# Kernel optimization log

Hardware: AMD Instinct MI355X
Metric: run time of the kernel (lower is better)

## Reference

```python
import jax, jax.numpy as jnp
import numpy as np

B, L = 8, 128
STATE_DIM, ACT_DIM = 6, 3
E = 256
D_MODEL = 256
N_LAYER = 4
D_INNER = 512   # expand=2
D_STATE = 16
DT_RANK = 16    # ceil(d_model/16)
D_CONV = 4
MAX_EP_LEN = 300
EPS = 1e-5


def rmsnorm(x, w):
    return x * jax.lax.rsqrt(jnp.mean(x * x, axis=-1, keepdims=True) + EPS) * w


def mamba_mixer(x, in_W, conv_w, conv_b, xproj_W, dt_W, dt_b, A_log, Dp, out_W):
    # x: (B, Lp, D_MODEL)
    bsz, Lp, _ = x.shape
    di = conv_w.shape[0]
    n = A_log.shape[-1]
    rk = dt_W.shape[0]
    xz = x @ in_W                              # (B, Lp, 2*di)
    xc, z = jnp.split(xz, 2, axis=-1)
    # depthwise causal conv1d, kernel D_CONV
    xc_t = xc.transpose(0, 2, 1)               # (B, di, Lp)
    xc_t = jax.lax.conv_general_dilated(
        xc_t, conv_w[:, None, :], (1,), [(D_CONV - 1, 0)],
        feature_group_count=di,
        dimension_numbers=('NCH', 'OIH', 'NCH')) + conv_b[None, :, None]
    xc = jax.nn.silu(xc_t.transpose(0, 2, 1))  # (B, Lp, di)
    proj = xc @ xproj_W                        # (B, Lp, rk + 2n)
    dt, Bm, Cm = jnp.split(proj, [rk, rk + n], axis=-1)
    dt = jax.nn.softplus(dt @ dt_W + dt_b)     # (B, Lp, di)
    A = -jnp.exp(A_log)                        # (di, n)

    def step(h, inp):
        dt_t, B_t, C_t, x_t = inp              # (B,di),(B,n),(B,n),(B,di)
        dA = jnp.exp(dt_t[:, :, None] * A)     # (B, di, n)
        h = dA * h + (dt_t * x_t)[:, :, None] * B_t[:, None, :]
        y = jnp.einsum('bdn,bn->bd', h, C_t)
        return h, y

    h0 = jnp.zeros((bsz, di, n), x.dtype)
    _, ys = jax.lax.scan(step, h0, (dt.transpose(1, 0, 2), Bm.transpose(1, 0, 2),
                                    Cm.transpose(1, 0, 2), xc.transpose(1, 0, 2)))
    y = ys.transpose(1, 0, 2) + xc * Dp        # (B, Lp, di)
    y = y * jax.nn.silu(z)
    return y @ out_W


def setup_inputs():
    key = jax.random.key(0)
    ks = jax.random.split(key, 24)
    s = 0.05
    inp = {}
    inp['states'] = jax.random.normal(ks[0], (B, L, STATE_DIM), jnp.float32)
    inp['actions'] = jax.random.normal(ks[1], (B, L, ACT_DIM), jnp.float32)
    inp['goal'] = jax.random.normal(ks[2], (B, L, STATE_DIM), jnp.float32)
    inp['timesteps'] = jax.random.randint(ks[3], (B, L), 0, MAX_EP_LEN)
    inp['te_W'] = jax.random.normal(ks[4], (MAX_EP_LEN, E)) * 0.02
    inp['se_W'] = jax.random.normal(ks[5], (STATE_DIM, E)) * s
    inp['se_b'] = jnp.zeros((E,))
    inp['ge_W'] = jax.random.normal(ks[6], (STATE_DIM, E)) * s
    inp['ge_b'] = jnp.zeros((E,))
    inp['ae_W'] = jax.random.normal(ks[7], (ACT_DIM, E)) * s
    inp['ae_b'] = jnp.zeros((E,))
    inp['bb_in_W'] = jax.random.normal(ks[8], (E, D_MODEL)) * s
    inp['bb_in_b'] = jnp.zeros((D_MODEL,))
    inp['norm_w'] = jnp.ones((N_LAYER, D_MODEL))
    inp['in_proj_W'] = jax.random.normal(ks[9], (N_LAYER, D_MODEL, 2 * D_INNER)) * s
    inp['conv_w'] = jax.random.normal(ks[10], (N_LAYER, D_INNER, D_CONV)) * s
    inp['conv_b'] = jnp.zeros((N_LAYER, D_INNER))
    inp['xproj_W'] = jax.random.normal(ks[11], (N_LAYER, D_INNER, DT_RANK + 2 * D_STATE)) * s
    inp['dt_W'] = jax.random.normal(ks[12], (N_LAYER, DT_RANK, D_INNER)) * s
    inp['dt_b'] = jnp.full((N_LAYER, D_INNER), float(np.log(np.expm1(0.01))), jnp.float32)
    inp['A_log'] = jnp.log(jnp.tile(jnp.arange(1, D_STATE + 1, dtype=jnp.float32), (N_LAYER, D_INNER, 1)))
    inp['Dp'] = jnp.ones((N_LAYER, D_INNER))
    inp['out_W'] = jax.random.normal(ks[13], (N_LAYER, D_INNER, D_MODEL)) * s / np.sqrt(N_LAYER)
    inp['fnorm_w'] = jnp.ones((D_MODEL,))
    inp['ps_W'] = jax.random.normal(ks[14], (D_MODEL, STATE_DIM)) * s
    inp['ps_b'] = jnp.zeros((STATE_DIM,))
    inp['pa_W'] = jax.random.normal(ks[15], (D_MODEL, ACT_DIM)) * s
    inp['pa_b'] = jnp.zeros((ACT_DIM,))
    return inp


def reference(states, actions, goal, timesteps, te_W, se_W, se_b, ge_W, ge_b,
              ae_W, ae_b, bb_in_W, bb_in_b, norm_w, in_proj_W, conv_w, conv_b,
              xproj_W, dt_W, dt_b, A_log, Dp, out_W, fnorm_w, ps_W, ps_b, pa_W, pa_b):
    bsz, Ls, _ = states.shape
    se = states @ se_W + se_b
    ge = goal @ ge_W + ge_b
    ae = actions @ ae_W + ae_b
    te = te_W[timesteps]                       # (B, L, E)
    se = se + te
    ae = ae + te
    ge = ge + te
    # interleave (g, s, a) per timestep -> (B, 3L, E)
    u = jnp.stack((ge, se, ae), axis=1).transpose(0, 2, 1, 3).reshape(bsz, 3 * Ls, E)
    residual = u @ bb_in_W + bb_in_b
    for i in range(norm_w.shape[0]):
        xn = rmsnorm(residual, norm_w[i])
        residual = residual + mamba_mixer(xn, in_proj_W[i], conv_w[i], conv_b[i],
                                          xproj_W[i], dt_W[i], dt_b[i], A_log[i],
                                          Dp[i], out_W[i])
    y = rmsnorm(residual, fnorm_w)
    y = y.reshape(bsz, Ls, 3, y.shape[-1]).transpose(0, 2, 1, 3)  # (B, 3, L, D)
    state_preds = y[:, -1] @ ps_W + ps_b       # from action-slot tokens
    action_preds = jnp.tanh(y[:, -2] @ pa_W + pa_b)  # from state-slot tokens
    return (state_preds, action_preds)
```

## Files before the change

### kernel.cpp

```cpp
#include <hip/hip_runtime.h>
#include <hip/hip_bf16.h>
#include <math.h>

#define BB 8
#define LL 128
#define SS 384
#define BT 3072
#define EE 256
#define DM 256
#define DI 512
#define DSTATE 16
#define RK 16
#define NL 4

typedef unsigned short u16;
typedef __attribute__((ext_vector_type(8))) short short8;
typedef __attribute__((ext_vector_type(4))) float f32x4;

__device__ __forceinline__ float bf(const u16 v){
    union { unsigned u; float f; } c; c.u = ((unsigned)v) << 16; return c.f;
}
__device__ __forceinline__ u16 f2bf(float f){
    union { float f; unsigned u; } c; c.f = f;
    unsigned x = c.u;
    unsigned r = (x >> 16) & 1u;
    x += 0x7fffu + r;
    return (u16)(x >> 16);
}
__device__ __forceinline__ unsigned pack2(float a, float b){
    return ((unsigned)f2bf(a)) | (((unsigned)f2bf(b)) << 16);
}

__global__ void k_probe(const unsigned* __restrict__ norm_w_raw, int* __restrict__ flag){
    if (threadIdx.x == 0 && blockIdx.x == 0){
        *flag = (norm_w_raw[0] == 0x3F800000u) ? 0 : 1;
    }
}

struct CvtArgs {
    const void* src[27];
    int n[27];
    int off[27];
};

__global__ __launch_bounds__(256) void k_convert(CvtArgs a, const int* __restrict__ flag,
                                                 float* __restrict__ dst){
    const int f = *flag;
    const int stride = gridDim.x * blockDim.x;
    const int tid0 = blockIdx.x * blockDim.x + threadIdx.x;
    #pragma unroll 1
    for (int s = 0; s < 27; ++s){
        const int n = a.n[s];
        float* d = dst + a.off[s];
        if (f){
            const u16* p = (const u16*)a.src[s];
            for (int i = tid0; i < n; i += stride) d[i] = bf(p[i]);
        } else {
            const float* p = (const float*)a.src[s];
            for (int i = tid0; i < n; i += stride) d[i] = p[i];
        }
    }
}

struct SwzDesc { const float* src; u16* dst; int K; int N; int frags; };
struct SwzArgs { SwzDesc d[13]; };

__global__ __launch_bounds__(256) void k_swz(SwzArgs a){
    int gid = blockIdx.x*256 + threadIdx.x;
    #pragma unroll 1
    for (int s = 0; s < 13; ++s){
        int f = a.d[s].frags;
        if (gid < f){
            const float* src = a.d[s].src;
            const int K = a.d[s].K, N = a.d[s].N;
            const int l = gid & 63;
            const int rest = gid >> 6;
            const int kcn = K >> 5;
            const int kc = rest % kcn;
            const int nt = rest / kcn;
            const int n  = nt*16 + (l & 15);
            const int k0 = kc*32 + (l >> 4)*8;
            u16 tmp[8];
            #pragma unroll
            for (int j = 0; j < 8; ++j) tmp[j] = f2bf(src[(size_t)(k0+j)*N + n]);
            *(short8*)(a.d[s].dst + (size_t)gid*8) = *(short8*)tmp;
            return;
        }
        gid -= f;
    }
}

__global__ __launch_bounds__(256) void k_embed_mfma(
    const float* __restrict__ states, const float* __restrict__ actions,
    const float* __restrict__ goal, const int* __restrict__ tsteps,
    const float* __restrict__ te_W, const float* __restrict__ se_W, const float* __restrict__ se_b,
    const float* __restrict__ ge_W, const float* __restrict__ ge_b,
    const float* __restrict__ ae_W, const float* __restrict__ ae_b,
    const u16* __restrict__ bbsw, const float* __restrict__ bb_b,
    float* __restrict__ residual)
{
    __shared__ u16 sA[32*264];
    const int tid = threadIdx.x;
    {
        const int m = tid >> 3, p = tid & 7, e0 = p*32;
        const int token = blockIdx.x*32 + m;
        const int b = token / SS, t = token % SS;
        const int slot = t % 3, step = t / 3;
        const int ts = tsteps[b*LL + step];
        float v[32];
        const float* tp = te_W + ts*EE + e0;
        #pragma unroll
        for (int i = 0; i < 8; ++i) *(float4*)(&v[i*4]) = *(const float4*)(tp + i*4);
        const float *bias, *Wp, *g; int nk;
        if (slot == 0){ bias = ge_b; Wp = ge_W; g = goal    + (b*LL+step)*6; nk = 6; }
        else if (slot == 1){ bias = se_b; Wp = se_W; g = states + (b*LL+step)*6; nk = 6; }
        else { bias = ae_b; Wp = ae_W; g = actions + (b*LL+step)*3; nk = 3; }
        #pragma unroll
        for (int i = 0; i < 8; ++i){
            float4 bv = *(const float4*)(bias + e0 + i*4);
            v[i*4]+=bv.x; v[i*4+1]+=bv.y; v[i*4+2]+=bv.z; v[i*4+3]+=bv.w;
        }
        for (int k = 0; k < nk; ++k){
            float gv = g[k];
            const float* wr = Wp + k*EE + e0;
            #pragma unroll
            for (int i = 0; i < 8; ++i){
                float4 wv = *(const float4*)(wr + i*4);
                v[i*4]+=gv*wv.x; v[i*4+1]+=gv*wv.y; v[i*4+2]+=gv*wv.z; v[i*4+3]+=gv*wv.w;
            }
        }
        unsigned* dp = (unsigned*)sA + (m*264 + e0)/2;
        #pragma unroll
        for (int i = 0; i < 16; ++i) dp[i] = pack2(v[2*i], v[2*i+1]);
    }
    __syncthreads();
    const int w = tid >> 6, l = tid & 63;
    const int mt = w >> 1, nq = w & 1;
    f32x4 acc[4] = {{0,0,0,0},{0,0,0,0},{0,0,0,0},{0,0,0,0}};
    const u16* ap0 = sA + (mt*16 + (l&15))*264 + (l>>4)*8;
    #pragma unroll
    for (int kc = 0; kc < 8; ++kc){
        short8 a = *(const short8*)(ap0 + kc*32);
        #pragma unroll
        for (int nt = 0; nt < 4; ++nt){
            int ntg = blockIdx.y*8 + nq*4 + nt;
            short8 b8 = *(const short8*)(bbsw + ((size_t)(ntg*8 + kc)*64 + l)*8);
            acc[nt] = __builtin_amdgcn_mfma_f32_16x16x32_bf16(a, b8, acc[nt], 0,0,0);
        }
    }
    const int mrow0 = blockIdx.x*32 + mt*16 + (l>>4)*4;
    #pragma unroll
    for (int nt = 0; nt < 4; ++nt){
        int col = (blockIdx.y*8 + nq*4 + nt)*16 + (l&15);
        float bb = bb_b[col];
        #pragma unroll
        for (int r = 0; r < 4; ++r)
            residual[(mrow0+r)*DM + col] = acc[nt][r] + bb;
    }
}

__global__ __launch_bounds__(256) void k_rms_inproj_mfma(
    const float* __restrict__ residual, const float* __restrict__ norm_w,
    const u16* __restrict__ Wsw,
    float* __restrict__ xc_raw, float* __restrict__ sz)
{
    __shared__ u16 sA[32*264];
    const int tid = threadIdx.x;
    {
        const int m = tid >> 3, p = tid & 7, e0 = p*32;
        const int row = blockIdx.x*32 + m;
        float v[32];
        const float* rp = residual + row*DM + e0;
        #pragma unroll
        for (int i = 0; i < 8; ++i) *(float4*)(&v[i*4]) = *(const float4*)(rp + i*4);
        float s = 0.f;
        #pragma unroll
        for (int i = 0; i < 32; ++i) s += v[i]*v[i];
        s += __shfl_xor(s,1,64); s += __shfl_xor(s,2,64); s += __shfl_xor(s,4,64);
        const float scale = rsqrtf(s*(1.f/DM) + 1e-5f);
        const float* nwp = norm_w + e0;
        unsigned* dp = (unsigned*)sA + (m*264 + e0)/2;
        #pragma unroll
        for (int i = 0; i < 16; ++i)
            dp[i] = pack2(v[2*i]*scale*nwp[2*i], v[2*i+1]*scale*nwp[2*i+1]);
    }
    __syncthreads();
    const int w = tid >> 6, l = tid & 63;
    const int mt = w >> 1, nq = w & 1;
    f32x4 acc[4] = {{0,0,0,0},{0,0,0,0},{0,0,0,0},{0,0,0,0}};
    const u16* ap0 = sA + (mt*16 + (l&15))*264 + (l>>4)*8;
    #pragma unroll
    for (int kc = 0; kc < 8; ++kc){
        short8 a = *(const short8*)(ap0 + kc*32);
        #pragma unroll
        for (int nt = 0; nt < 4; ++nt){
            int ntg = blockIdx.y*8 + nq*4 + nt;
            short8 b8 = *(const short8*)(Wsw + ((size_t)(ntg*8 + kc)*64 + l)*8);
            acc[nt] = __builtin_amdgcn_mfma_f32_16x16x32_bf16(a, b8, acc[nt], 0,0,0);
        }
    }
    const int mrow0 = blockIdx.x*32 + mt*16 + (l>>4)*4;
    if (blockIdx.y < 4){
        #pragma unroll
        for (int nt = 0; nt < 4; ++nt){
            int col = (blockIdx.y*8 + nq*4 + nt)*16 + (l&15);
            #pragma unroll
            for (int r = 0; r < 4; ++r)
                xc_raw[(mrow0+r)*DI + col] = acc[nt][r];
        }
    } else {
        #pragma unroll
        for (int nt = 0; nt < 4; ++nt){
            int col = (blockIdx.y*8 + nq*4 + nt)*16 + (l&15) - DI;
            #pragma unroll
            for (int r = 0; r < 4; ++r){
                float z = acc[nt][r];
                sz[(mrow0+r)*DI + col] = z / (1.f + __expf(-z));
            }
        }
    }
}

__global__ __launch_bounds__(256) void k_conv_mfma(
    const float* __restrict__ xc_raw,
    const float* __restrict__ conv_w, const float* __restrict__ conv_b,
    const u16* __restrict__ xpsw,
    const float* __restrict__ dt_W, const float* __restrict__ dt_b,
    float* __restrict__ xc, float* __restrict__ dtBC, float* __restrict__ dt)
{
    __shared__ u16 sxc[16*520];
    __shared__ float sdtbc[16*64];
    const int tid = threadIdx.x;
    const int base = blockIdx.x * 16;
    const int t0 = base % SS;

    #pragma unroll
    for (int half = 0; half < 2; ++half){
        const int d = tid + half*256;
        const float w0 = conv_w[d*4+0], w1 = conv_w[d*4+1];
        const float w2 = conv_w[d*4+2], w3 = conv_w[d*4+3];
        const float cb = conv_b[d];
        const float* rp = xc_raw + (size_t)base*DI + d;
        float xm3=0.f, xm2=0.f, xm1=0.f;
        if (t0 > 0){
            xm3 = rp[-3*DI]; xm2 = rp[-2*DI]; xm1 = rp[-DI];
        }
        #pragma unroll
        for (int tk = 0; tk < 16; ++tk){
            float x0 = rp[tk*DI];
            float a = cb + w0*xm3 + w1*xm2 + w2*xm1 + w3*x0;
            float s = a / (1.f + __expf(-a));
            xc[(size_t)(base+tk)*DI + d] = s;
            sxc[tk*520 + d] = f2bf(s);
            xm3 = xm2; xm2 = xm1; xm1 = x0;
        }
    }
    __syncthreads();

    const int w = tid >> 6, l = tid & 63;
    if (w < 3){
        f32x4 acc = {0,0,0,0};
        const u16* ap0 = sxc + (l&15)*520 + (l>>4)*8;
        #pragma unroll
        for (int kc = 0; kc < 16; ++kc){
            short8 a = *(const short8*)(ap0 + kc*32);
            short8 b8 = *(const short8*)(xpsw + ((size_t)(w*16 + kc)*64 + l)*8);
            acc = __builtin_amdgcn_mfma_f32_16x16x32_bf16(a, b8, acc, 0,0,0);
        }
        #pragma unroll
        for (int r = 0; r < 4; ++r)
            sdtbc[((l>>4)*4 + r)*64 + w*16 + (l&15)] = acc[r];
    }
    __syncthreads();

    #pragma unroll
    for (int r = 0; r < 2; ++r){
        int i = tid + r*256;
        int t = i >> 5, j = i & 31;
        dtBC[(size_t)(base+t)*48 + 16 + j] = sdtbc[t*64 + 16 + j];
    }

    #pragma unroll
    for (int half = 0; half < 2; ++half){
        const int d = tid + half*256;
        const float db = dt_b[d];
        float wr[16];
        #pragma unroll
        for (int r = 0; r < 16; ++r) wr[r] = dt_W[r*DI + d];
        #pragma unroll
        for (int tk = 0; tk < 16; ++tk){
            float a = db;
            #pragma unroll
            for (int r = 0; r < 16; ++r) a += sdtbc[tk*64 + r] * wr[r];
            float sp = (a > 15.f) ? a : __logf(1.f + __expf(a));
            dt[(size_t)(base+tk)*DI + d] = sp;
        }
    }
}

#define CT 32
#define NCH (SS/CT)

__global__ __launch_bounds__(256) void k_scan(
    const float* __restrict__ dt, const float* __restrict__ dtBC,
    const float* __restrict__ xc,
    const float* __restrict__ A_log, const float* __restrict__ Dp,
    float* __restrict__ y)
{
    __shared__ float s_dt[2][CT*16];
    __shared__ float s_xc[2][CT*16];
    __shared__ float s_B [2][CT*16];
    __shared__ float s_C [2][CT*16];
    __shared__ float s_p [CT*16*17];
    __shared__ float s_Dp[16];

    const int tid = threadIdx.x;
    const int bk  = blockIdx.x;
    const int b   = bk >> 5;
    const int dg  = bk & 31;
    const int dgb = dg*16;
    const int ld  = tid >> 4, n = tid & 15;
    const int d   = dgb + ld;

    const float A = -__expf(A_log[d*DSTATE + n]);
    const size_t tokbase = (size_t)b*SS;

    float r_dt[2], r_xc[2], r_bc[4];

    auto issue_loads = [&](int c){
        const int t0 = c*CT;
        #pragma unroll
        for (int r = 0; r < 2; ++r){
            int e = tid + r*256;
            int t = e >> 4, dd = e & 15;
            size_t g = (tokbase + t0 + t)*DI + dgb + dd;
            r_dt[r] = dt[g];
            r_xc[r] = xc[g];
        }
        #pragma unroll
        for (int r = 0; r < 4; ++r){
            int e = tid + r*256;
            int t = e >> 5, j = e & 31;
            r_bc[r] = dtBC[(tokbase + t0 + t)*48 + 16 + j];
        }
    };
    auto commit = [&](int bu){
        #pragma unroll
        for (int r = 0; r < 2; ++r){
            int e = tid + r*256;
            s_dt[bu][e] = r_dt[r];
            s_xc[bu][e] = r_xc[r];
        }
        #pragma unroll
        for (int r = 0; r < 4; ++r){
            int e = tid + r*256;
            int t = e >> 5, j = e & 31;
            if (j < 16) s_B[bu][t*16 + j]      = r_bc[r];
            else        s_C[bu][t*16 + (j-16)] = r_bc[r];
        }
    };

    issue_loads(0);
    commit(0);
    if (tid < 16) s_Dp[tid] = Dp[dgb + tid];

    float h = 0.f;
    int buf = 0;
    for (int c = 0; c < NCH; ++c){
        __syncthreads();
        if (c+1 < NCH) issue_loads(c+1);
        const float* pdt = s_dt[buf];
        const float* pxc = s_xc[buf];
        const float* pB  = s_B[buf];
        const float* pC  = s_C[buf];
        float* pp = s_p + ld*17 + n;
        #pragma unroll
        for (int t = 0; t < CT; ++t){
            float dtv = pdt[t*16 + ld];
            float xv  = pxc[t*16 + ld];
            float Bv  = pB [t*16 + n];
            float dA  = __expf(dtv * A);
            h = dA*h + (dtv*xv)*Bv;
            pp[t*272] = h * pC[t*16 + n];
        }
        __syncthreads();
        {
            const int t0 = c*CT;
            #pragma unroll
            for (int r = 0; r < 2; ++r){
                int e = tid + r*256;
                int t = e >> 4, dd = e & 15;
                const float* q = s_p + e*17;
                float s = 0.f;
                #pragma unroll
                for (int k = 0; k < 16; ++k) s += q[k];
                y[(tokbase + t0 + t)*DI + dgb + dd] = s + pxc[e]*s_Dp[dd];
            }
        }
        if (c+1 < NCH) commit(buf^1);
        buf ^= 1;
    }
}

__global__ __launch_bounds__(256) void k_outproj_mfma(
    const float* __restrict__ y, const float* __restrict__ szb,
    const u16* __restrict__ Wsw, float* __restrict__ residual)
{
    __shared__ u16 sA[16*520];
    const int tid = threadIdx.x;
    {
        const int m = tid >> 4, p = tid & 15, e0 = p*32;
        const int row = blockIdx.x*16 + m;
        const float* yp = y   + (size_t)row*DI + e0;
        const float* sp = szb + (size_t)row*DI + e0;
        unsigned* dp = (unsigned*)sA + (m*520 + e0)/2;
        #pragma unroll
        for (int i = 0; i < 8; ++i){
            float4 yv = *(const float4*)(yp + i*4);
            float4 sv = *(const float4*)(sp + i*4);
            dp[i*2]   = pack2(yv.x*sv.x, yv.y*sv.y);
            dp[i*2+1] = pack2(yv.z*sv.z, yv.w*sv.w);
        }
    }
    __syncthreads();
    const int w = tid >> 6, l = tid & 63;
    f32x4 acc[2] = {{0,0,0,0},{0,0,0,0}};
    const u16* ap0 = sA + (l&15)*520 + (l>>4)*8;
    #pragma unroll
    for (int kc = 0; kc < 16; ++kc){
        short8 a = *(const short8*)(ap0 + kc*32);
        #pragma unroll
        for (int i = 0; i < 2; ++i){
            int ntg = blockIdx.y*8 + w*2 + i;
            short8 b8 = *(const short8*)(Wsw + ((size_t)(ntg*16 + kc)*64 + l)*8);
            acc[i] = __builtin_amdgcn_mfma_f32_16x16x32_bf16(a, b8, acc[i], 0,0,0);
        }
    }
    const int mrow0 = blockIdx.x*16 + (l>>4)*4;
    #pragma unroll
    for (int i = 0; i < 2; ++i){
        int col = (blockIdx.y*8 + w*2 + i)*16 + (l&15);
        #pragma unroll
        for (int r = 0; r < 4; ++r)
            residual[(mrow0+r)*DM + col] += acc[i][r];
    }
}

__global__ __launch_bounds__(256) void k_heads(
    const float* __restrict__ residual, const float* __restrict__ fnorm_w,
    const float* __restrict__ ps_W, const float* __restrict__ ps_b,
    const float* __restrict__ pa_W, const float* __restrict__ pa_b,
    const int* __restrict__ flag, void* __restrict__ out)
{
    __shared__ float x1[DM], x2[DM];
    __shared__ float sc[2];
    __shared__ float part[2][4];
    const int tid = threadIdx.x;
    const int bl = blockIdx.x;
    const int b = bl >> 7, l = bl & 127;
    const int fl = *flag;
    const int tok1 = b*SS + 3*l + 1;
    const int tok2 = tok1 + 1;
    float v1 = residual[tok1*DM + tid];
    float v2 = residual[tok2*DM + tid];
    {
        float s1 = v1*v1, s2 = v2*v2;
        #pragma unroll
        for (int off = 32; off >= 1; off >>= 1){
            s1 += __shfl_xor(s1, off, 64);
            s2 += __shfl_xor(s2, off, 64);
        }
        if ((tid & 63) == 0){ part[0][tid>>6] = s1; part[1][tid>>6] = s2; }
    }
    __syncthreads();
    if (tid < 2){
        float s = part[tid][0]+part[tid][1]+part[tid][2]+part[tid][3];
        sc[tid] = rsqrtf(s * (1.f/DM) + 1e-5f);
    }
    __syncthreads();
    float nw = fnorm_w[tid];
    x1[tid] = v1 * sc[0] * nw;
    x2[tid] = v2 * sc[1] * nw;
    __syncthreads();
    const int wv = tid >> 6, ln = tid & 63;
    for (int oi = wv; oi < 9; oi += 4){
        float a = 0.f;
        if (oi < 6){
            #pragma unroll
            for (int k = 0; k < 4; ++k){ int e = ln + 64*k; a += x2[e] * ps_W[e*6 + oi]; }
        } else {
            int j = oi - 6;
            #pragma unroll
            for (int k = 0; k < 4; ++k){ int e = ln + 64*k; a += x1[e] * pa_W[e*3 + j]; }
        }
        #pragma unroll
        for (int off = 32; off >= 1; off >>= 1) a += __shfl_xor(a, off, 64);
        if (ln == 0){
            float r; int idx;
            if (oi < 6){
                r = a + ps_b[oi];
                idx = (b*LL + l)*6 + oi;
            } else {
                int j = oi - 6;
                r = tanhf(a + pa_b[j]);
                idx = BB*LL*6 + (b*LL + l)*3 + j;
            }
            if (fl) ((u16*)out)[idx] = f2bf(r);
            else    ((float*)out)[idx] = r;
        }
    }
}

extern "C" void kernel_launch(void* const* d_in, const int* in_sizes, int n_in,
                              void* d_out, int out_size, void* d_ws, size_t ws_size,
                              hipStream_t stream)
{
    const int* tsteps = (const int*)d_in[3];

    int* flag = (int*)d_ws;
    float* fin = ((float*)d_ws) + 16;

    const int fidx[27] = {0,1,2,4,5,6,7,8,9,10,11,12,13,14,15,16,17,18,19,20,
                          21,22,23,24,25,26,27};
    CvtArgs ca;
    const float* fp[28];
    int cur = 0;
    for (int i = 0; i < 27; ++i){
        int gi = fidx[i];
        ca.src[i] = d_in[gi];
        ca.n[i]   = in_sizes[gi];
        ca.off[i] = cur;
        fp[gi] = fin + cur;
        cur += in_sizes[gi];
        cur = (cur + 3) & ~3;
    }
    float* act = fin + cur;

    float* residual = act;            act += BT*DM;
    float* xc_raw   = act;            act += BT*DI;
    float* sz       = act;            act += BT*DI;
    float* xc       = act;            act += BT*DI;
    float* dtbuf    = act;            act += BT*DI;
    float* ybuf     = act;            act += BT*DI;
    float* dtBC     = act;            act += BT*48;

    u16* wsb    = (u16*)act;
    u16* bb_sw  = wsb;
    u16* in_sw  = bb_sw + 65536;
    u16* out_sw = in_sw + 4*262144;
    u16* xp_sw  = out_sw + 4*131072;

    k_probe<<<1, 64, 0, stream>>>((const unsigned*)d_in[13], flag);
    k_convert<<<512, 256, 0, stream>>>(ca, flag, fin);

    SwzArgs sa;
    sa.d[0] = { fp[11], bb_sw, 256, 256, (256/16)*(256/32)*64 };
    for (int i = 0; i < 4; ++i)
        sa.d[1+i] = { fp[14] + i*DM*2*DI, in_sw + i*262144, 256, 1024,
                      (1024/16)*(256/32)*64 };
    for (int i = 0; i < 4; ++i)
        sa.d[5+i] = { fp[22] + i*DI*DM, out_sw + i*131072, 512, 256,
                      (256/16)*(512/32)*64 };
    for (int i = 0; i < 4; ++i)
        sa.d[9+i] = { fp[17] + i*DI*48, xp_sw + i*24576, 512, 48,
                      (48/16)*(512/32)*64 };
    int total_frags = 8192 + 4*32768 + 4*16384 + 4*3072;
    k_swz<<<total_frags/256, 256, 0, stream>>>(sa);

    k_embed_mfma<<<dim3(96,2), 256, 0, stream>>>(fp[0], fp[1], fp[2], tsteps,
        fp[4], fp[5], fp[6], fp[7], fp[8], fp[9], fp[10], bb_sw, fp[12], residual);

    for (int lyr = 0; lyr < NL; ++lyr){
        k_rms_inproj_mfma<<<dim3(96,8), 256, 0, stream>>>(residual, fp[13] + lyr*DM,
            in_sw + lyr*262144, xc_raw, sz);
        k_conv_mfma<<<BT/16, 256, 0, stream>>>(xc_raw, fp[15] + lyr*DI*4,
            fp[16] + lyr*DI, xp_sw + lyr*24576, fp[18] + lyr*RK*DI, fp[19] + lyr*DI,
            xc, dtBC, dtbuf);
        k_scan<<<256, 256, 0, stream>>>(dtbuf, dtBC, xc,
            fp[20] + lyr*DI*DSTATE, fp[21] + lyr*DI, ybuf);
        k_outproj_mfma<<<dim3(192,2), 256, 0, stream>>>(ybuf, sz,
            out_sw + lyr*131072, residual);
    }
    k_heads<<<BB*LL, 256, 0, stream>>>(residual, fp[23], fp[24], fp[25], fp[26], fp[27],
                                       flag, (u16*)d_out);
}
```

Before: 384.3 us.

## Fuse prep kernels and fold next-layer RMSNorm+in_proj into out_proj

Merges the dtype probe, input conversion and weight swizzle into one prep kernel. The swizzle now reads raw inputs directly, so weight matrices no longer get a separate fp32 conversion pass. The out-projection kernel now also applies the next layer's RMSNorm and in_proj (with SiLU on z) on its 16-row tile, which removes three inproj launches and a residual re-read. The scan stores dt and dt*x interleaved so the inner loop does one float2 load and one fewer multiply. The cost is that the fused kernel runs only 192 blocks for the full 1024-wide in_proj, so it has less parallelism than the separate 768-block launch.

```diff
diff --git a/kernel.cpp b/kernel.cpp
--- a/kernel.cpp
+++ b/kernel.cpp
@@ -30,63 +30,73 @@
 __device__ __forceinline__ unsigned pack2(float a, float b){
     return ((unsigned)f2bf(a)) | (((unsigned)f2bf(b)) << 16);
 }
-
-__global__ void k_probe(const unsigned* __restrict__ norm_w_raw, int* __restrict__ flag){
-    if (threadIdx.x == 0 && blockIdx.x == 0){
-        *flag = (norm_w_raw[0] == 0x3F800000u) ? 0 : 1;
-    }
-}
-
-struct CvtArgs {
-    const void* src[27];
-    int n[27];
-    int off[27];
+__device__ __forceinline__ int get_flag(const unsigned* nwraw){
+    return (nwraw[0] == 0x3F800000u) ? 0 : 1;
+}
+
+#define SWZ_NB 848
+#define CNV_NB 64
+
+__device__ __constant__ int g_soff[13] = {0, 0, 262144, 524288, 786432,
+                                          0, 131072, 262144, 393216,
+                                          0, 24576, 49152, 73728};
+
+struct SwzDesc { const void* src; u16* dst; int K; int N; int frags; };
+struct PrepArgs {
+    const void* csrc[23]; int cn[23]; int coff[23];
+    SwzDesc sd[13];
 };
 
-__global__ __launch_bounds__(256) void k_convert(CvtArgs a, const int* __restrict__ flag,
-                                                 float* __restrict__ dst){
-    const int f = *flag;
-    const int stride = gridDim.x * blockDim.x;
-    const int tid0 = blockIdx.x * blockDim.x + threadIdx.x;
-    #pragma unroll 1
-    for (int s = 0; s < 27; ++s){
-        const int n = a.n[s];
-        float* d = dst + a.off[s];
-        if (f){
-            const u16* p = (const u16*)a.src[s];
-            for (int i = tid0; i < n; i += stride) d[i] = bf(p[i]);
-        } else {
-            const float* p = (const float*)a.src[s];
-            for (int i = tid0; i < n; i += stride) d[i] = p[i];
-        }
-    }
-}
-
-struct SwzDesc { const float* src; u16* dst; int K; int N; int frags; };
-struct SwzArgs { SwzDesc d[13]; };
-
-__global__ __launch_bounds__(256) void k_swz(SwzArgs a){
-    int gid = blockIdx.x*256 + threadIdx.x;
-    #pragma unroll 1
-    for (int s = 0; s < 13; ++s){
-        int f = a.d[s].frags;
-        if (gid < f){
-            const float* src = a.d[s].src;
-            const int K = a.d[s].K, N = a.d[s].N;
-            const int l = gid & 63;
-            const int rest = gid >> 6;
-            const int kcn = K >> 5;
-            const int kc = rest % kcn;
-            const int nt = rest / kcn;
-            const int n  = nt*16 + (l & 15);
-            const int k0 = kc*32 + (l >> 4)*8;
-            u16 tmp[8];
-            #pragma unroll
-            for (int j = 0; j < 8; ++j) tmp[j] = f2bf(src[(size_t)(k0+j)*N + n]);
-            *(short8*)(a.d[s].dst + (size_t)gid*8) = *(short8*)tmp;
-            return;
-        }
-        gid -= f;
+__global__ __launch_bounds__(256) void k_prep(PrepArgs a,
+                                              const unsigned* __restrict__ nwraw,
+                                              float* __restrict__ dst){
+    const int f = get_flag(nwraw);
+    const int bk = blockIdx.x;
+    if (bk < SWZ_NB){
+        int gid = bk*256 + threadIdx.x;
+        #pragma unroll 1
+        for (int s = 0; s < 13; ++s){
+            int fr = a.sd[s].frags;
+            if (gid < fr){
+                const int N = a.sd[s].N;
+                const int l = gid & 63;
+                const int rest = gid >> 6;
+                const int kcn = a.sd[s].K >> 5;
+                const int kc = rest % kcn;
+                const int nt = rest / kcn;
+                const int n  = nt*16 + (l & 15);
+                const int k0 = kc*32 + (l >> 4)*8;
+                u16 tmp[8];
+                if (f){
+                    const u16* src = (const u16*)a.sd[s].src;
+                    #pragma unroll
+                    for (int j = 0; j < 8; ++j) tmp[j] = src[(size_t)(k0+j)*N + n];
+                } else {
+                    const float* src = (const float*)((const char*)a.sd[s].src
+                                                      + (size_t)g_soff[s]*2);
+                    #pragma unroll
+                    for (int j = 0; j < 8; ++j) tmp[j] = f2bf(src[(size_t)(k0+j)*N + n]);
+                }
+                *(short8*)(a.sd[s].dst + (size_t)gid*8) = *(short8*)tmp;
+                return;
+            }
+            gid -= fr;
+        }
+    } else {
+        const int stride = CNV_NB * 256;
+        const int tid0 = (bk - SWZ_NB)*256 + threadIdx.x;
+        #pragma unroll 1
+        for (int s = 0; s < 23; ++s){
+            const int n = a.cn[s];
+            float* d = dst + a.coff[s];
+            if (f){
+                const u16* p = (const u16*)a.csrc[s];
+                for (int i = tid0; i < n; i += stride) d[i] = bf(p[i]);
+            } else {
+                const float* p = (const float*)a.csrc[s];
+                for (int i = tid0; i < n; i += stride) d[i] = p[i];
+            }
+        }
     }
 }
 
@@ -307,8 +317,8 @@
     const float* __restrict__ A_log, const float* __restrict__ Dp,
     float* __restrict__ y)
 {
-    __shared__ float s_dt[2][CT*16];
-    __shared__ float s_xc[2][CT*16];
+    __shared__ float s_dtx[2][CT*32];
+    __shared__ float s_xc [2][CT*16];
     __shared__ float s_B [2][CT*16];
     __shared__ float s_C [2][CT*16];
     __shared__ float s_p [CT*16*17];
@@ -348,7 +358,9 @@
         #pragma unroll
         for (int r = 0; r < 2; ++r){
             int e = tid + r*256;
-            s_dt[bu][e] = r_dt[r];
+            int t = e >> 4, dd = e & 15;
+            s_dtx[bu][t*32 + dd*2]     = r_dt[r];
+            s_dtx[bu][t*32 + dd*2 + 1] = r_dt[r]*r_xc[r];
             s_xc[bu][e] = r_xc[r];
         }
         #pragma unroll
@@ -369,23 +381,22 @@
     for (int c = 0; c < NCH; ++c){
         __syncthreads();
         if (c+1 < NCH) issue_loads(c+1);
-        const float* pdt = s_dt[buf];
-        const float* pxc = s_xc[buf];
+        const float* pdx = s_dtx[buf] + ld*2;
         const float* pB  = s_B[buf];
         const float* pC  = s_C[buf];
         float* pp = s_p + ld*17 + n;
         #pragma unroll
         for (int t = 0; t < CT; ++t){
-            float dtv = pdt[t*16 + ld];
-            float xv  = pxc[t*16 + ld];
-            float Bv  = pB [t*16 + n];
-            float dA  = __expf(dtv * A);
-            h = dA*h + (dtv*xv)*Bv;
+            float2 dx = *(const float2*)(pdx + t*32);
+            float Bv  = pB[t*16 + n];
+            float dA  = __expf(dx.x * A);
+            h = dA*h + dx.y*Bv;
             pp[t*272] = h * pC[t*16 + n];
         }
         __syncthreads();
         {
             const int t0 = c*CT;
+            const float* pxc = s_xc[buf];
             #pragma unroll
             for (int r = 0; r < 2; ++r){
                 int e = tid + r*256;
@@ -402,17 +413,21 @@
     }
 }
 
-__global__ __launch_bounds__(256) void k_outproj_mfma(
+__global__ __launch_bounds__(256) void k_out_rms(
     const float* __restrict__ y, const float* __restrict__ szb,
-    const u16* __restrict__ Wsw, float* __restrict__ residual)
+    const u16* __restrict__ Wout, float* __restrict__ residual,
+    const float* __restrict__ norm_w, const u16* __restrict__ Win,
+    float* __restrict__ xc_raw, float* __restrict__ sz,
+    int do_rms)
 {
     __shared__ u16 sA[16*520];
+    __shared__ float sRes[16*264];
     const int tid = threadIdx.x;
+    const int base = blockIdx.x*16;
     {
         const int m = tid >> 4, p = tid & 15, e0 = p*32;
-        const int row = blockIdx.x*16 + m;
-        const float* yp = y   + (size_t)row*DI + e0;
-        const float* sp = szb + (size_t)row*DI + e0;
+        const float* yp = y   + (size_t)(base+m)*DI + e0;
+        const float* sp = szb + (size_t)(base+m)*DI + e0;
         unsigned* dp = (unsigned*)sA + (m*520 + e0)/2;
         #pragma unroll
         for (int i = 0; i < 8; ++i){
@@ -424,25 +439,81 @@
     }
     __syncthreads();
     const int w = tid >> 6, l = tid & 63;
-    f32x4 acc[2] = {{0,0,0,0},{0,0,0,0}};
-    const u16* ap0 = sA + (l&15)*520 + (l>>4)*8;
-    #pragma unroll
-    for (int kc = 0; kc < 16; ++kc){
-        short8 a = *(const short8*)(ap0 + kc*32);
-        #pragma unroll
-        for (int i = 0; i < 2; ++i){
-            int ntg = blockIdx.y*8 + w*2 + i;
-            short8 b8 = *(const short8*)(Wsw + ((size_t)(ntg*16 + kc)*64 + l)*8);
-            acc[i] = __builtin_amdgcn_mfma_f32_16x16x32_bf16(a, b8, acc[i], 0,0,0);
-        }
-    }
-    const int mrow0 = blockIdx.x*16 + (l>>4)*4;
-    #pragma unroll
-    for (int i = 0; i < 2; ++i){
-        int col = (blockIdx.y*8 + w*2 + i)*16 + (l&15);
-        #pragma unroll
-        for (int r = 0; r < 4; ++r)
-            residual[(mrow0+r)*DM + col] += acc[i][r];
+    {
+        f32x4 acc[4] = {{0,0,0,0},{0,0,0,0},{0,0,0,0},{0,0,0,0}};
+        const u16* ap0 = sA + (l&15)*520 + (l>>4)*8;
+        #pragma unroll
+        for (int kc = 0; kc < 16; ++kc){
+            short8 a = *(const short8*)(ap0 + kc*32);
+            #pragma unroll
+            for (int i = 0; i < 4; ++i){
+                int ntg = w*4 + i;
+                short8 b8 = *(const short8*)(Wout + ((size_t)(ntg*16 + kc)*64 + l)*8);
+                acc[i] = __builtin_amdgcn_mfma_f32_16x16x32_bf16(a, b8, acc[i], 0,0,0);
+            }
+        }
+        const int mrow0 = (l>>4)*4;
+        #pragma unroll
+        for (int i = 0; i < 4; ++i){
+            int col = (w*4+i)*16 + (l&15);
+            #pragma unroll
+            for (int r = 0; r < 4; ++r){
+                float v = residual[(base+mrow0+r)*DM + col] + acc[i][r];
+                residual[(base+mrow0+r)*DM + col] = v;
+                if (do_rms) sRes[(mrow0+r)*264 + col] = v;
+            }
+        }
+    }
+    if (!do_rms) return;
+    __syncthreads();
+    {
+        const int m = tid >> 4, p = tid & 15;
+        const float* rr = sRes + m*264 + p*16;
+        float v[16];
+        float ss = 0.f;
+        #pragma unroll
+        for (int i = 0; i < 16; ++i){ v[i] = rr[i]; ss += v[i]*v[i]; }
+        ss += __shfl_xor(ss,1,64); ss += __shfl_xor(ss,2,64);
+        ss += __shfl_xor(ss,4,64); ss += __shfl_xor(ss,8,64);
+        const float scale = rsqrtf(ss*(1.f/DM) + 1e-5f);
+        const float* nw = norm_w + p*16;
+        unsigned* dp = (unsigned*)sA + (m*264 + p*16)/2;
+        #pragma unroll
+        for (int i = 0; i < 8; ++i)
+            dp[i] = pack2(v[2*i]*scale*nw[2*i], v[2*i+1]*scale*nw[2*i+1]);
+    }
+    __syncthreads();
+    {
+        f32x4 acc[16];
+        #pragma unroll
+        for (int i = 0; i < 16; ++i) acc[i] = {0,0,0,0};
+        const u16* ap0 = sA + (l&15)*264 + (l>>4)*8;
+        #pragma unroll
+        for (int kc = 0; kc < 8; ++kc){
+            short8 a = *(const short8*)(ap0 + kc*32);
+            #pragma unroll
+            for (int i = 0; i < 16; ++i){
+                int ntg = w*16 + i;
+                short8 b8 = *(const short8*)(Win + ((size_t)(ntg*8 + kc)*64 + l)*8);
+                acc[i] = __builtin_amdgcn_mfma_f32_16x16x32_bf16(a, b8, acc[i], 0,0,0);
+            }
+        }
+        const int mrow0 = (l>>4)*4;
+        #pragma unroll
+        for (int i = 0; i < 16; ++i){
+            int col = (w*16+i)*16 + (l&15);
+            if (col < DI){
+                #pragma unroll
+                for (int r = 0; r < 4; ++r)
+                    xc_raw[(size_t)(base+mrow0+r)*DI + col] = acc[i][r];
+            } else {
+                #pragma unroll
+                for (int r = 0; r < 4; ++r){
+                    float z = acc[i][r];
+                    sz[(size_t)(base+mrow0+r)*DI + col - DI] = z / (1.f + __expf(-z));
+                }
+            }
+        }
     }
 }
 
@@ -450,7 +521,7 @@
     const float* __restrict__ residual, const float* __restrict__ fnorm_w,
     const float* __restrict__ ps_W, const float* __restrict__ ps_b,
     const float* __restrict__ pa_W, const float* __restrict__ pa_b,
-    const int* __restrict__ flag, void* __restrict__ out)
+    const unsigned* __restrict__ nwraw, void* __restrict__ out)
 {
     __shared__ float x1[DM], x2[DM];
     __shared__ float sc[2];
@@ -458,7 +529,7 @@
     const int tid = threadIdx.x;
     const int bl = blockIdx.x;
     const int b = bl >> 7, l = bl & 127;
-    const int fl = *flag;
+    const int fl = get_flag(nwraw);
     const int tok1 = b*SS + 3*l + 1;
     const int tok2 = tok1 + 1;
     float v1 = residual[tok1*DM + tid];
@@ -516,20 +587,20 @@
                               hipStream_t stream)
 {
     const int* tsteps = (const int*)d_in[3];
-
-    int* flag = (int*)d_ws;
-    float* fin = ((float*)d_ws) + 16;
-
-    const int fidx[27] = {0,1,2,4,5,6,7,8,9,10,11,12,13,14,15,16,17,18,19,20,
-                          21,22,23,24,25,26,27};
-    CvtArgs ca;
+    const unsigned* nwraw = (const unsigned*)d_in[13];
+
+    float* fin = (float*)d_ws;
+
+    const int cidx[23] = {0,1,2,4,5,6,7,8,9,10,12,13,15,16,18,19,20,21,23,24,25,26,27};
+    PrepArgs pa;
     const float* fp[28];
+    for (int i = 0; i < 28; ++i) fp[i] = nullptr;
     int cur = 0;
-    for (int i = 0; i < 27; ++i){
-        int gi = fidx[i];
-        ca.src[i] = d_in[gi];
-        ca.n[i]   = in_sizes[gi];
-        ca.off[i] = cur;
+    for (int i = 0; i < 23; ++i){
+        int gi = cidx[i];
+        pa.csrc[i] = d_in[gi];
+        pa.cn[i]   = in_sizes[gi];
+        pa.coff[i] = cur;
         fp[gi] = fin + cur;
         cur += in_sizes[gi];
         cur = (cur + 3) & ~3;
@@ -550,37 +621,45 @@
     u16* out_sw = in_sw + 4*262144;
     u16* xp_sw  = out_sw + 4*131072;
 
-    k_probe<<<1, 64, 0, stream>>>((const unsigned*)d_in[13], flag);
-    k_convert<<<512, 256, 0, stream>>>(ca, flag, fin);
-
-    SwzArgs sa;
-    sa.d[0] = { fp[11], bb_sw, 256, 256, (256/16)*(256/32)*64 };
+    const int soff[13] = {0, 0, 262144, 524288, 786432,
+                          0, 131072, 262144, 393216,
+                          0, 24576, 49152, 73728};
+    pa.sd[0] = { d_in[11], bb_sw, 256, 256, (256/16)*(256/32)*64 };
     for (int i = 0; i < 4; ++i)
-        sa.d[1+i] = { fp[14] + i*DM*2*DI, in_sw + i*262144, 256, 1024,
-                      (1024/16)*(256/32)*64 };
+        pa.sd[1+i] = { d_in[14], in_sw + i*262144, 256, 1024,
+                       (1024/16)*(256/32)*64 };
     for (int i = 0; i < 4; ++i)
-        sa.d[5+i] = { fp[22] + i*DI*DM, out_sw + i*131072, 512, 256,
-                      (256/16)*(512/32)*64 };
+        pa.sd[5+i] = { d_in[22], out_sw + i*131072, 512, 256,
+                       (256/16)*(512/32)*64 };
     for (int i = 0; i < 4; ++i)
-        sa.d[9+i] = { fp[17] + i*DI*48, xp_sw + i*24576, 512, 48,
-                      (48/16)*(512/32)*64 };
-    int total_frags = 8192 + 4*32768 + 4*16384 + 4*3072;
-    k_swz<<<total_frags/256, 256, 0, stream>>>(sa);
+        pa.sd[9+i] = { d_in[17], xp_sw + i*24576, 512, 48,
+                       (48/16)*(512/32)*64 };
+    for (int i = 0; i < 13; ++i)
+        pa.sd[i].src = (const void*)((const char*)pa.sd[i].src + (size_t)soff[i]*2);
+
+    k_prep<<<SWZ_NB + CNV_NB, 256, 0, stream>>>(pa, nwraw, fin);
 
     k_embed_mfma<<<dim3(96,2), 256, 0, stream>>>(fp[0], fp[1], fp[2], tsteps,
         fp[4], fp[5], fp[6], fp[7], fp[8], fp[9], fp[10], bb_sw, fp[12], residual);
 
+    k_rms_inproj_mfma<<<dim3(96,8), 256, 0, stream>>>(residual, fp[13],
+        in_sw, xc_raw, sz);
+
     for (int lyr = 0; lyr < NL; ++lyr){
-        k_rms_inproj_mfma<<<dim3(96,8), 256, 0, stream>>>(residual, fp[13] + lyr*DM,
-            in_sw + lyr*262144, xc_raw, sz);
         k_conv_mfma<<<BT/16, 256, 0, stream>>>(xc_raw, fp[15] + lyr*DI*4,
             fp[16] + lyr*DI, xp_sw + lyr*24576, fp[18] + lyr*RK*DI, fp[19] + lyr*DI,
             xc, dtBC, dtbuf);
         k_scan<<<256, 256, 0, stream>>>(dtbuf, dtBC, xc,
             fp[20] + lyr*DI*DSTATE, fp[21] + lyr*DI, ybuf);
-        k_outproj_mfma<<<dim3(192,2), 256, 0, stream>>>(ybuf, sz,
-            out_sw + lyr*131072, residual);
+        if (lyr < NL-1){
+            k_out_rms<<<192, 256, 0, stream>>>(ybuf, sz, out_sw + lyr*131072,
+                residual, fp[13] + (lyr+1)*DM, in_sw + (lyr+1)*262144,
+                xc_raw, sz, 1);
+        } else {
+            k_out_rms<<<192, 256, 0, stream>>>(ybuf, sz, out_sw + lyr*131072,
+                residual, fp[13], in_sw, xc_raw, sz, 0);
+        }
     }
     k_heads<<<BB*LL, 256, 0, stream>>>(residual, fp[23], fp[24], fp[25], fp[26], fp[27],
-                                       flag, (u16*)d_out);
-}
+                                       nwraw, (u16*)d_out);
+}
```

Measured after the change: 448.8 us. +16.8%, slower.
